# Kernel optimization log

Hardware: AMD Instinct MI355X
Metric: run time of the kernel (lower is better)

The kernel has to match this reference:

```python
import jax, jax.numpy as jnp
import numpy as np

D_MODEL = 1024
N_HEADS = 16
D_HEAD = D_MODEL // N_HEADS


def setup_inputs() -> dict:
    key = jax.random.key(0)
    ks = jax.random.split(key, 5)
    s_in = 1.0 / np.sqrt(D_MODEL)
    x = jax.random.normal(ks[0], (2, 2048, D_MODEL), dtype=jnp.float32)
    W_qkv = jax.random.uniform(ks[1], (D_MODEL, 3 * D_MODEL), jnp.float32, -s_in, s_in)
    b_qkv = jax.random.uniform(ks[2], (3 * D_MODEL,), jnp.float32, -s_in, s_in)
    W_out = jax.random.uniform(ks[3], (D_MODEL, D_MODEL), jnp.float32, -s_in, s_in)
    b_out = jax.random.uniform(ks[4], (D_MODEL,), jnp.float32, -s_in, s_in)
    return {"x": x, "W_qkv": W_qkv, "b_qkv": b_qkv, "W_out": W_out, "b_out": b_out}


def reference(x, W_qkv, b_qkv, W_out, b_out):
    B, T, C = x.shape
    qkv = x @ W_qkv + b_qkv                      # [B,T,3C]
    q, k, v = jnp.split(qkv, 3, axis=-1)
    # [B,T,C] -> [B,H,T,Dh]
    def heads(t):
        return t.reshape(B, T, N_HEADS, D_HEAD).transpose(0, 2, 1, 3)
    q, k, v = heads(q), heads(k), heads(v)
    att = jnp.einsum('bhqd,bhkd->bhqk', q, k) / np.sqrt(D_HEAD).astype(np.float32)
    causal = jnp.tril(jnp.ones((T, T), dtype=bool))  # True = keep
    att = jnp.where(causal, att, -jnp.inf)
    att = jax.nn.softmax(att, axis=-1)
    y = jnp.einsum('bhqk,bhkd->bhqd', att, v)    # [B,H,T,Dh]
    y = y.transpose(0, 2, 1, 3).reshape(B, T, C)
    y = y @ W_out + b_out
    return (y, att)
```

## Files before the change

kernel.cpp:

```cpp
#include <hip/hip_runtime.h>

#define B_ 2
#define T_ 2048
#define C_ 1024
#define H_ 16
#define DH_ 64
#define N3_ 3072
#define BT_ 4096

typedef __attribute__((ext_vector_type(4))) float f32x4;
typedef __attribute__((ext_vector_type(8))) short short8;
typedef __attribute__((ext_vector_type(4))) unsigned short us4;

__device__ __forceinline__ unsigned short f2bf(float f) {
  return __builtin_bit_cast(unsigned short, (__bf16)f);
}

__device__ __forceinline__ float bf2f(unsigned short s) {
  unsigned int u = ((unsigned int)s) << 16;
  return __builtin_bit_cast(float, u);
}

__device__ __forceinline__ void gload16(const void* g, void* l) {
  __builtin_amdgcn_global_load_lds(
      (const __attribute__((address_space(1))) unsigned int*)g,
      (__attribute__((address_space(3))) unsigned int*)l, 16, 0, 0);
}

__device__ __forceinline__ void lds_barrier() {
  asm volatile("s_waitcnt lgkmcnt(0)" ::: "memory");
  __builtin_amdgcn_s_barrier();
}

#define VM_BARRIER(N)                                        \
  do {                                                       \
    asm volatile("s_waitcnt vmcnt(" #N ")" ::: "memory");    \
    __builtin_amdgcn_s_barrier();                            \
  } while (0)

#define QSCALE 0.1803368801111137f

__global__ __launch_bounds__(256) void prep_kernel(const float* __restrict__ x,
                                                   const float* __restrict__ W_qkv,
                                                   const float* __restrict__ W_out,
                                                   unsigned short* __restrict__ xb,
                                                   unsigned short* __restrict__ wqkvT,
                                                   unsigned short* __restrict__ woutT) {
  __shared__ float tile[32][33];
  int b = blockIdx.x;
  if (b < 4096) {
    size_t i = (size_t)b * 256 + threadIdx.x;
    float4 v = *(const float4*)(x + i * 4);
    us4 o = {f2bf(v.x), f2bf(v.y), f2bf(v.z), f2bf(v.w)};
    *(us4*)(xb + i * 4) = o;
    return;
  }
  const float* W;
  unsigned short* Wt;
  int Ncols, bx, by;
  if (b < 4096 + 3072) {
    int bb = b - 4096;
    W = W_qkv; Wt = wqkvT; Ncols = 3072; bx = bb % 96; by = bb / 96;
  } else {
    int bb = b - 7168;
    W = W_out; Wt = woutT; Ncols = 1024; bx = bb % 32; by = bb / 32;
  }
  int n0 = bx * 32, k0 = by * 32;
  int tx = threadIdx.x & 31, ty = threadIdx.x >> 5;
#pragma unroll
  for (int i = 0; i < 4; ++i) {
    int k = k0 + ty + i * 8;
    tile[ty + i * 8][tx] = W[(size_t)k * Ncols + n0 + tx];
  }
  __syncthreads();
#pragma unroll
  for (int i = 0; i < 4; ++i) {
    int n = n0 + ty + i * 8;
    Wt[(size_t)n * 1024 + k0 + tx] = f2bf(tile[tx][ty + i * 8]);
  }
}

template <int MODE, int BN>
__global__ __launch_bounds__(256) void gemm_kernel(
    const unsigned short* __restrict__ A, const unsigned short* __restrict__ Bt,
    const float* __restrict__ bias, unsigned short* __restrict__ q_ws,
    unsigned short* __restrict__ k_ws, unsigned short* __restrict__ vt_ws,
    float* __restrict__ yout) {
  __shared__ unsigned short lds_a[128 * 32];
  __shared__ unsigned short lds_b[BN * 32];
  const int tid = threadIdx.x;
  const int w = tid >> 6, l = tid & 63;
  const int m0 = blockIdx.y * 128;
  const int n0 = blockIdx.x * BN;
  const int wr = (w >> 1) * 64, wc = (w & 1) * (BN / 2);
  constexpr int NI = BN / 32;
  const int K = 1024;

  f32x4 acc[4][NI] = {};
  for (int k0 = 0; k0 < K; k0 += 32) {
    __syncthreads();
#pragma unroll
    for (int i = 0; i < 2; ++i) {
      int li = i * 256 + tid;
      int row = li >> 2, cl = li & 3, cs = cl ^ (row & 3);
      gload16((const char*)A + ((size_t)(m0 + row) * K + k0) * 2 + cs * 16,
              (char*)lds_a + li * 16);
    }
#pragma unroll
    for (int i = 0; i < BN / 64; ++i) {
      int li = i * 256 + tid;
      int row = li >> 2, cl = li & 3, cs = cl ^ (row & 3);
      gload16((const char*)Bt + ((size_t)(n0 + row) * K + k0) * 2 + cs * 16,
              (char*)lds_b + li * 16);
    }
    __syncthreads();
    short8 af[4], bfr[NI];
#pragma unroll
    for (int mi = 0; mi < 4; ++mi) {
      int m = wr + mi * 16 + (l & 15);
      af[mi] = *(const short8*)((const char*)lds_a + m * 64 + (((l >> 4) ^ (m & 3)) * 16));
    }
#pragma unroll
    for (int ni = 0; ni < NI; ++ni) {
      int n = wc + ni * 16 + (l & 15);
      bfr[ni] = *(const short8*)((const char*)lds_b + n * 64 + (((l >> 4) ^ (n & 3)) * 16));
    }
#pragma unroll
    for (int mi = 0; mi < 4; ++mi)
#pragma unroll
      for (int ni = 0; ni < NI; ++ni)
        acc[mi][ni] = __builtin_amdgcn_mfma_f32_16x16x32_bf16(af[mi], bfr[ni], acc[mi][ni], 0, 0, 0);
  }

  float bi[NI];
#pragma unroll
  for (int ni = 0; ni < NI; ++ni) bi[ni] = bias[n0 + wc + ni * 16 + (l & 15)];

  if (MODE == 1) {
#pragma unroll
    for (int mi = 0; mi < 4; ++mi) {
#pragma unroll
      for (int ni = 0; ni < NI; ++ni) {
        int n = n0 + wc + ni * 16 + (l & 15);
#pragma unroll
        for (int r = 0; r < 4; ++r) {
          int m = m0 + wr + mi * 16 + ((l >> 4) << 2) + r;
          yout[(size_t)m * 1024 + n] = acc[mi][ni][r] + bi[ni];
        }
      }
    }
  } else {
    int sec = (n0 + wc) >> 10;
#pragma unroll
    for (int mi = 0; mi < 4; ++mi) {
#pragma unroll
      for (int ni = 0; ni < NI; ++ni) {
        int n = n0 + wc + ni * 16 + (l & 15);
        int nn = n & 1023, h = nn >> 6, d = nn & 63;
        if (sec == 2) {
          int mbase = m0 + wr + mi * 16 + ((l >> 4) << 2);
          int bb = mbase >> 11, t = mbase & 2047;
          us4 o;
#pragma unroll
          for (int r = 0; r < 4; ++r) o[r] = f2bf(acc[mi][ni][r] + bi[ni]);
          *(us4*)(vt_ws + ((size_t)(bb * 16 + h) * 64 + d) * 2048 + t) = o;
        } else {
#pragma unroll
          for (int r = 0; r < 4; ++r) {
            int m = m0 + wr + mi * 16 + ((l >> 4) << 2) + r;
            int bb = m >> 11, t = m & 2047;
            float v = acc[mi][ni][r] + bi[ni];
            size_t idx = ((size_t)(bb * 16 + h) * 2048 + t) * 64 + d;
            if (sec == 0)
              q_ws[idx] = f2bf(v * QSCALE);
            else
              k_ws[idx] = f2bf(v);
          }
        }
      }
    }
  }
}

__global__ __launch_bounds__(512) void attn_kernel(
    const unsigned short* __restrict__ q_ws, const unsigned short* __restrict__ k_ws,
    const unsigned short* __restrict__ vt_ws, float* __restrict__ att,
    unsigned short* __restrict__ yh) {
  __shared__ unsigned short lds_k[2][64 * 64];
  __shared__ unsigned short lds_v[2][64 * 64];
  __shared__ unsigned short lds_p[128 * 72];
  const int tid = threadIdx.x, w = tid >> 6, l = tid & 63;
  const int id = blockIdx.x;
  const int rr = id >> 8, j = id & 255;
  int qt = j & 15;
  if (rr) qt = 15 - qt;
  const int bh = (j >> 4) + (rr << 4);
  const int q0 = qt * 128;
  const size_t hoff = (size_t)bh * (2048 * 64);
  const char* kbase = (const char*)k_ws + hoff * 2;
  const char* vbase = (const char*)vt_ws + hoff * 2;

  auto stageK = [&](int kt, int buf) {
    int row = tid >> 3, cl = tid & 7, cs = cl ^ (row & 7);
    gload16(kbase + (size_t)kt * 8192 + row * 128 + cs * 16, (char*)lds_k[buf] + tid * 16);
  };
  auto stageV = [&](int kt, int buf) {
    int row = tid >> 3, cl = tid & 7, cs = cl ^ (row & 7);
    gload16(vbase + (size_t)row * 4096 + kt * 128 + cs * 16, (char*)lds_v[buf] + tid * 16);
  };

  short8 qf[2];
  {
    int row = q0 + w * 16 + (l & 15);
    const char* qb = (const char*)q_ws + (hoff + (size_t)row * 64) * 2;
    qf[0] = *(const short8*)(qb + ((l >> 4) * 16));
    qf[1] = *(const short8*)(qb + 64 + ((l >> 4) * 16));
  }

  const int rowbase = q0 + w * 16 + ((l >> 4) << 2);
  const int nkt = 2 * qt + 2;

  float lsum[4] = {0.f, 0.f, 0.f, 0.f};
  stageK(0, 0);
  VM_BARRIER(0);
  for (int kt = 0; kt < nkt; ++kt) {
    const int cur = kt & 1;
    if (kt + 1 < nkt) stageK(kt + 1, cur ^ 1);
    const bool diag = (kt >= 2 * qt);
    f32x4 s[4] = {};
    __builtin_amdgcn_s_setprio(1);
#pragma unroll
    for (int ni = 0; ni < 4; ++ni) {
      int jj = ni * 16 + (l & 15);
#pragma unroll
      for (int cc = 0; cc < 2; ++cc) {
        short8 bf = *(const short8*)((const char*)lds_k[cur] + jj * 128 +
                                     (((cc * 4 + (l >> 4)) ^ (jj & 7)) * 16));
        s[ni] = __builtin_amdgcn_mfma_f32_16x16x32_bf16(qf[cc], bf, s[ni], 0, 0, 0);
      }
    }
    __builtin_amdgcn_s_setprio(0);
#pragma unroll
    for (int ni = 0; ni < 4; ++ni) {
#pragma unroll
      for (int r = 0; r < 4; ++r) {
        float e = __builtin_exp2f(s[ni][r]);
        if (diag) {
          int colg = kt * 64 + ni * 16 + (l & 15);
          if (colg > rowbase + r) e = 0.f;
        }
        lsum[r] += e;
      }
    }
    if (kt + 1 < nkt) VM_BARRIER(0);
  }

  float invl[4];
#pragma unroll
  for (int r = 0; r < 4; ++r) {
    float t = lsum[r];
    t += __shfl_xor(t, 1);
    t += __shfl_xor(t, 2);
    t += __shfl_xor(t, 4);
    t += __shfl_xor(t, 8);
    invl[r] = 1.0f / t;
  }

  f32x4 yacc[4] = {};
  float* attb = att + (size_t)bh * 2048 * 2048;
  stageK(0, 0);
  stageV(0, 0);
  VM_BARRIER(0);
  for (int kt = 0; kt < nkt; ++kt) {
    const int cur = kt & 1;
    if (kt + 1 < nkt) { stageK(kt + 1, cur ^ 1); stageV(kt + 1, cur ^ 1); }
    const bool diag = (kt >= 2 * qt);
    f32x4 s[4] = {};
    __builtin_amdgcn_s_setprio(1);
#pragma unroll
    for (int ni = 0; ni < 4; ++ni) {
      int jj = ni * 16 + (l & 15);
#pragma unroll
      for (int cc = 0; cc < 2; ++cc) {
        short8 bf = *(const short8*)((const char*)lds_k[cur] + jj * 128 +
                                     (((cc * 4 + (l >> 4)) ^ (jj & 7)) * 16));
        s[ni] = __builtin_amdgcn_mfma_f32_16x16x32_bf16(qf[cc], bf, s[ni], 0, 0, 0);
      }
    }
    __builtin_amdgcn_s_setprio(0);
#pragma unroll
    for (int ni = 0; ni < 4; ++ni) {
#pragma unroll
      for (int r = 0; r < 4; ++r) {
        float p = __builtin_exp2f(s[ni][r]) * invl[r];
        if (diag) {
          int colg = kt * 64 + ni * 16 + (l & 15);
          if (colg > rowbase + r) p = 0.f;
        }
        lds_p[(w * 16 + ((l >> 4) << 2) + r) * 72 + ni * 16 + (l & 15)] = f2bf(p);
      }
    }
    lds_barrier();
#pragma unroll
    for (int cc = 0; cc < 2; ++cc) {
      int prow = w * 16 + (l & 15);
      short8 pf = *(const short8*)((const char*)lds_p + prow * 144 + cc * 64 + ((l >> 4) * 16));
      float* ad = attb + (size_t)(q0 + prow) * 2048 + kt * 64 + cc * 32 + ((l >> 4) * 8);
      float4 v0 = make_float4(bf2f((unsigned short)pf[0]), bf2f((unsigned short)pf[1]),
                              bf2f((unsigned short)pf[2]), bf2f((unsigned short)pf[3]));
      float4 v1 = make_float4(bf2f((unsigned short)pf[4]), bf2f((unsigned short)pf[5]),
                              bf2f((unsigned short)pf[6]), bf2f((unsigned short)pf[7]));
      *(float4*)ad = v0;
      *(float4*)(ad + 4) = v1;
      __builtin_amdgcn_s_setprio(1);
#pragma unroll
      for (int ni = 0; ni < 4; ++ni) {
        int d = ni * 16 + (l & 15);
        short8 vf = *(const short8*)((const char*)lds_v[cur] + d * 128 +
                                     (((cc * 4 + (l >> 4)) ^ (d & 7)) * 16));
        yacc[ni] = __builtin_amdgcn_mfma_f32_16x16x32_bf16(pf, vf, yacc[ni], 0, 0, 0);
      }
      __builtin_amdgcn_s_setprio(0);
    }
    if (kt + 1 < nkt) VM_BARRIER(4);
  }

  {
    int bb = bh >> 4, h = bh & 15;
#pragma unroll
    for (int ni = 0; ni < 4; ++ni) {
      int d = ni * 16 + (l & 15);
#pragma unroll
      for (int r = 0; r < 4; ++r) {
        int t = rowbase + r;
        yh[((size_t)bb * 2048 + t) * 1024 + h * 64 + d] = f2bf(yacc[ni][r]);
      }
    }
  }

  int cstart = q0 + 128;
  if (cstart < 2048) {
    int nz = 2048 - cstart;
    float4 z = make_float4(0.f, 0.f, 0.f, 0.f);
    for (int row = 0; row < 128; ++row) {
      float* dst = attb + (size_t)(q0 + row) * 2048 + cstart;
      for (int c = tid * 4; c < nz; c += 2048) *(float4*)(dst + c) = z;
    }
  }
}

extern "C" void kernel_launch(void* const* d_in, const int* in_sizes, int n_in,
                              void* d_out, int out_size, void* d_ws, size_t ws_size,
                              hipStream_t stream) {
  const float* x = (const float*)d_in[0];
  const float* W_qkv = (const float*)d_in[1];
  const float* b_qkv = (const float*)d_in[2];
  const float* W_out = (const float*)d_in[3];
  const float* b_out = (const float*)d_in[4];
  float* out = (float*)d_out;

  char* ws = (char*)d_ws;
  unsigned short* xb = (unsigned short*)(ws);
  unsigned short* wqkvT = (unsigned short*)(ws + 8388608);
  unsigned short* woutT = (unsigned short*)(ws + 14680064);
  unsigned short* q_ws = (unsigned short*)(ws + 16777216);
  unsigned short* k_ws = (unsigned short*)(ws + 25165824);
  unsigned short* vt_ws = (unsigned short*)(ws + 33554432);
  unsigned short* yh_ws = (unsigned short*)(ws + 41943040);

  float* y_out = out;
  float* att_out = out + (size_t)BT_ * C_;

  prep_kernel<<<8192, 256, 0, stream>>>(x, W_qkv, W_out, xb, wqkvT, woutT);
  gemm_kernel<0, 128><<<dim3(24, 32), 256, 0, stream>>>(xb, wqkvT, b_qkv, q_ws, k_ws, vt_ws,
                                                        nullptr);
  attn_kernel<<<512, 512, 0, stream>>>(q_ws, k_ws, vt_ws, att_out, yh_ws);
  gemm_kernel<1, 64><<<dim3(16, 32), 256, 0, stream>>>(yh_ws, woutT, b_out, nullptr, nullptr,
                                                       nullptr, y_out);
}
```

Before: 252.5 us.

## Split attention into stats and write kernels, use nontemporal stores for att

Moves the softmax row-sum pass into its own kernel that writes inverse row sums to workspace, reusing the xb region since it is dead after the QKV GEMM. The write kernel then loads those sums and does only the probability write and PV accumulation. Stores of the large attention matrix and its zero fill become nontemporal to avoid polluting cache. The split adds a kernel launch and a small global round trip but lets each kernel use fewer registers and less LDS.

```diff
diff --git a/kernel.cpp b/kernel.cpp
--- a/kernel.cpp
+++ b/kernel.cpp
@@ -182,10 +182,86 @@
   }
 }
 
-__global__ __launch_bounds__(512) void attn_kernel(
+__global__ __launch_bounds__(512) void attn_stats_kernel(
     const unsigned short* __restrict__ q_ws, const unsigned short* __restrict__ k_ws,
-    const unsigned short* __restrict__ vt_ws, float* __restrict__ att,
-    unsigned short* __restrict__ yh) {
+    float* __restrict__ invl_ws) {
+  __shared__ unsigned short lds_k[2][64 * 64];
+  const int tid = threadIdx.x, w = tid >> 6, l = tid & 63;
+  const int id = blockIdx.x;
+  const int rr = id >> 8, j = id & 255;
+  int qt = j & 15;
+  if (rr) qt = 15 - qt;
+  const int bh = (j >> 4) + (rr << 4);
+  const int q0 = qt * 128;
+  const size_t hoff = (size_t)bh * (2048 * 64);
+  const char* kbase = (const char*)k_ws + hoff * 2;
+
+  auto stageK = [&](int kt, int buf) {
+    int row = tid >> 3, cl = tid & 7, cs = cl ^ (row & 7);
+    gload16(kbase + (size_t)kt * 8192 + row * 128 + cs * 16, (char*)lds_k[buf] + tid * 16);
+  };
+
+  short8 qf[2];
+  {
+    int row = q0 + w * 16 + (l & 15);
+    const char* qb = (const char*)q_ws + (hoff + (size_t)row * 64) * 2;
+    qf[0] = *(const short8*)(qb + ((l >> 4) * 16));
+    qf[1] = *(const short8*)(qb + 64 + ((l >> 4) * 16));
+  }
+
+  const int rowbase = q0 + w * 16 + ((l >> 4) << 2);
+  const int nkt = 2 * qt + 2;
+
+  float lsum[4] = {0.f, 0.f, 0.f, 0.f};
+  stageK(0, 0);
+  VM_BARRIER(0);
+  for (int kt = 0; kt < nkt; ++kt) {
+    const int cur = kt & 1;
+    if (kt + 1 < nkt) stageK(kt + 1, cur ^ 1);
+    const bool diag = (kt >= 2 * qt);
+    f32x4 s[4] = {};
+    __builtin_amdgcn_s_setprio(1);
+#pragma unroll
+    for (int ni = 0; ni < 4; ++ni) {
+      int jj = ni * 16 + (l & 15);
+#pragma unroll
+      for (int cc = 0; cc < 2; ++cc) {
+        short8 bf = *(const short8*)((const char*)lds_k[cur] + jj * 128 +
+                                     (((cc * 4 + (l >> 4)) ^ (jj & 7)) * 16));
+        s[ni] = __builtin_amdgcn_mfma_f32_16x16x32_bf16(qf[cc], bf, s[ni], 0, 0, 0);
+      }
+    }
+    __builtin_amdgcn_s_setprio(0);
+#pragma unroll
+    for (int ni = 0; ni < 4; ++ni) {
+#pragma unroll
+      for (int r = 0; r < 4; ++r) {
+        float e = __builtin_exp2f(s[ni][r]);
+        if (diag) {
+          int colg = kt * 64 + ni * 16 + (l & 15);
+          if (colg > rowbase + r) e = 0.f;
+        }
+        lsum[r] += e;
+      }
+    }
+    if (kt + 1 < nkt) VM_BARRIER(0);
+  }
+
+#pragma unroll
+  for (int r = 0; r < 4; ++r) {
+    float t = lsum[r];
+    t += __shfl_xor(t, 1);
+    t += __shfl_xor(t, 2);
+    t += __shfl_xor(t, 4);
+    t += __shfl_xor(t, 8);
+    if ((l & 15) == 0) invl_ws[bh * 2048 + rowbase + r] = 1.0f / t;
+  }
+}
+
+__global__ __launch_bounds__(512) void attn_write_kernel(
+    const unsigned short* __restrict__ q_ws, const unsigned short* __restrict__ k_ws,
+    const unsigned short* __restrict__ vt_ws, const float* __restrict__ invl_ws,
+    float* __restrict__ att, unsigned short* __restrict__ yh) {
   __shared__ unsigned short lds_k[2][64 * 64];
   __shared__ unsigned short lds_v[2][64 * 64];
   __shared__ unsigned short lds_p[128 * 72];
@@ -220,51 +296,9 @@
   const int rowbase = q0 + w * 16 + ((l >> 4) << 2);
   const int nkt = 2 * qt + 2;
 
-  float lsum[4] = {0.f, 0.f, 0.f, 0.f};
-  stageK(0, 0);
-  VM_BARRIER(0);
-  for (int kt = 0; kt < nkt; ++kt) {
-    const int cur = kt & 1;
-    if (kt + 1 < nkt) stageK(kt + 1, cur ^ 1);
-    const bool diag = (kt >= 2 * qt);
-    f32x4 s[4] = {};
-    __builtin_amdgcn_s_setprio(1);
-#pragma unroll
-    for (int ni = 0; ni < 4; ++ni) {
-      int jj = ni * 16 + (l & 15);
-#pragma unroll
-      for (int cc = 0; cc < 2; ++cc) {
-        short8 bf = *(const short8*)((const char*)lds_k[cur] + jj * 128 +
-                                     (((cc * 4 + (l >> 4)) ^ (jj & 7)) * 16));
-        s[ni] = __builtin_amdgcn_mfma_f32_16x16x32_bf16(qf[cc], bf, s[ni], 0, 0, 0);
-      }
-    }
-    __builtin_amdgcn_s_setprio(0);
-#pragma unroll
-    for (int ni = 0; ni < 4; ++ni) {
-#pragma unroll
-      for (int r = 0; r < 4; ++r) {
-        float e = __builtin_exp2f(s[ni][r]);
-        if (diag) {
-          int colg = kt * 64 + ni * 16 + (l & 15);
-          if (colg > rowbase + r) e = 0.f;
-        }
-        lsum[r] += e;
-      }
-    }
-    if (kt + 1 < nkt) VM_BARRIER(0);
-  }
-
   float invl[4];
 #pragma unroll
-  for (int r = 0; r < 4; ++r) {
-    float t = lsum[r];
-    t += __shfl_xor(t, 1);
-    t += __shfl_xor(t, 2);
-    t += __shfl_xor(t, 4);
-    t += __shfl_xor(t, 8);
-    invl[r] = 1.0f / t;
-  }
+  for (int r = 0; r < 4; ++r) invl[r] = invl_ws[bh * 2048 + rowbase + r];
 
   f32x4 yacc[4] = {};
   float* attb = att + (size_t)bh * 2048 * 2048;
@@ -306,12 +340,12 @@
       int prow = w * 16 + (l & 15);
       short8 pf = *(const short8*)((const char*)lds_p + prow * 144 + cc * 64 + ((l >> 4) * 16));
       float* ad = attb + (size_t)(q0 + prow) * 2048 + kt * 64 + cc * 32 + ((l >> 4) * 8);
-      float4 v0 = make_float4(bf2f((unsigned short)pf[0]), bf2f((unsigned short)pf[1]),
-                              bf2f((unsigned short)pf[2]), bf2f((unsigned short)pf[3]));
-      float4 v1 = make_float4(bf2f((unsigned short)pf[4]), bf2f((unsigned short)pf[5]),
-                              bf2f((unsigned short)pf[6]), bf2f((unsigned short)pf[7]));
-      *(float4*)ad = v0;
-      *(float4*)(ad + 4) = v1;
+      f32x4 v0 = {bf2f((unsigned short)pf[0]), bf2f((unsigned short)pf[1]),
+                  bf2f((unsigned short)pf[2]), bf2f((unsigned short)pf[3])};
+      f32x4 v1 = {bf2f((unsigned short)pf[4]), bf2f((unsigned short)pf[5]),
+                  bf2f((unsigned short)pf[6]), bf2f((unsigned short)pf[7])};
+      __builtin_nontemporal_store(v0, (f32x4*)ad);
+      __builtin_nontemporal_store(v1, (f32x4*)(ad + 4));
       __builtin_amdgcn_s_setprio(1);
 #pragma unroll
       for (int ni = 0; ni < 4; ++ni) {
@@ -341,10 +375,11 @@
   int cstart = q0 + 128;
   if (cstart < 2048) {
     int nz = 2048 - cstart;
-    float4 z = make_float4(0.f, 0.f, 0.f, 0.f);
+    f32x4 z = {0.f, 0.f, 0.f, 0.f};
     for (int row = 0; row < 128; ++row) {
       float* dst = attb + (size_t)(q0 + row) * 2048 + cstart;
-      for (int c = tid * 4; c < nz; c += 2048) *(float4*)(dst + c) = z;
+      for (int c = tid * 4; c < nz; c += 2048)
+        __builtin_nontemporal_store(z, (f32x4*)(dst + c));
     }
   }
 }
@@ -361,6 +396,7 @@
 
   char* ws = (char*)d_ws;
   unsigned short* xb = (unsigned short*)(ws);
+  float* invl_ws = (float*)(ws);
   unsigned short* wqkvT = (unsigned short*)(ws + 8388608);
   unsigned short* woutT = (unsigned short*)(ws + 14680064);
   unsigned short* q_ws = (unsigned short*)(ws + 16777216);
@@ -374,7 +410,8 @@
   prep_kernel<<<8192, 256, 0, stream>>>(x, W_qkv, W_out, xb, wqkvT, woutT);
   gemm_kernel<0, 128><<<dim3(24, 32), 256, 0, stream>>>(xb, wqkvT, b_qkv, q_ws, k_ws, vt_ws,
                                                         nullptr);
-  attn_kernel<<<512, 512, 0, stream>>>(q_ws, k_ws, vt_ws, att_out, yh_ws);
+  attn_stats_kernel<<<512, 512, 0, stream>>>(q_ws, k_ws, invl_ws);
+  attn_write_kernel<<<512, 512, 0, stream>>>(q_ws, k_ws, vt_ws, invl_ws, att_out, yh_ws);
   gemm_kernel<1, 64><<<dim3(16, 32), 256, 0, stream>>>(yh_ws, woutT, b_out, nullptr, nullptr,
                                                        nullptr, y_out);
 }
```

Measured after the change: 324.4 us. +28.5%, slower.

## Use 128-wide single-buffered K/V tiles in attention instead of double-buffered 64-wide

Applied to the files above, without the earlier changes.

Widens the key tile from 64 to 128 columns so each iteration does twice the MFMA work and the loop runs half as many times. It drops the double-buffered prefetch: each iteration now barriers, loads K (and V), waits, then computes. This halves the per-tile loop and barrier count, but load latency is no longer hidden behind compute. The diagonal tile now masks more wasted work, and the P tile is written in two halves with an extra barrier.

```diff
diff --git a/kernel.cpp b/kernel.cpp
--- a/kernel.cpp
+++ b/kernel.cpp
@@ -186,8 +186,8 @@
     const unsigned short* __restrict__ q_ws, const unsigned short* __restrict__ k_ws,
     const unsigned short* __restrict__ vt_ws, float* __restrict__ att,
     unsigned short* __restrict__ yh) {
-  __shared__ unsigned short lds_k[2][64 * 64];
-  __shared__ unsigned short lds_v[2][64 * 64];
+  __shared__ unsigned short lds_k[128 * 64];
+  __shared__ unsigned short lds_v[64 * 128];
   __shared__ unsigned short lds_p[128 * 72];
   const int tid = threadIdx.x, w = tid >> 6, l = tid & 63;
   const int id = blockIdx.x;
@@ -200,13 +200,21 @@
   const char* kbase = (const char*)k_ws + hoff * 2;
   const char* vbase = (const char*)vt_ws + hoff * 2;
 
-  auto stageK = [&](int kt, int buf) {
-    int row = tid >> 3, cl = tid & 7, cs = cl ^ (row & 7);
-    gload16(kbase + (size_t)kt * 8192 + row * 128 + cs * 16, (char*)lds_k[buf] + tid * 16);
+  auto stageK = [&](int kt) {
+#pragma unroll
+    for (int i = 0; i < 2; ++i) {
+      int li = i * 512 + tid;
+      int row = li >> 3, cl = li & 7, cs = cl ^ (row & 7);
+      gload16(kbase + ((size_t)kt * 128 + row) * 128 + cs * 16, (char*)lds_k + li * 16);
+    }
   };
-  auto stageV = [&](int kt, int buf) {
-    int row = tid >> 3, cl = tid & 7, cs = cl ^ (row & 7);
-    gload16(vbase + (size_t)row * 4096 + kt * 128 + cs * 16, (char*)lds_v[buf] + tid * 16);
+  auto stageV = [&](int kt) {
+#pragma unroll
+    for (int i = 0; i < 2; ++i) {
+      int li = i * 512 + tid;
+      int row = li >> 4, cl = li & 15, cs = cl ^ (row & 15);
+      gload16(vbase + (size_t)row * 4096 + kt * 256 + cs * 16, (char*)lds_v + li * 16);
+    }
   };
 
   short8 qf[2];
@@ -218,41 +226,41 @@
   }
 
   const int rowbase = q0 + w * 16 + ((l >> 4) << 2);
-  const int nkt = 2 * qt + 2;
+  const int nkt = qt + 1;
 
   float lsum[4] = {0.f, 0.f, 0.f, 0.f};
-  stageK(0, 0);
-  VM_BARRIER(0);
   for (int kt = 0; kt < nkt; ++kt) {
-    const int cur = kt & 1;
-    if (kt + 1 < nkt) stageK(kt + 1, cur ^ 1);
-    const bool diag = (kt >= 2 * qt);
-    f32x4 s[4] = {};
+    lds_barrier();
+    stageK(kt);
+    VM_BARRIER(0);
+    const bool diag = (kt == qt);
+    f32x4 s[8];
+#pragma unroll
+    for (int ni = 0; ni < 8; ++ni) s[ni] = f32x4{0.f, 0.f, 0.f, 0.f};
     __builtin_amdgcn_s_setprio(1);
 #pragma unroll
-    for (int ni = 0; ni < 4; ++ni) {
+    for (int ni = 0; ni < 8; ++ni) {
       int jj = ni * 16 + (l & 15);
 #pragma unroll
       for (int cc = 0; cc < 2; ++cc) {
-        short8 bf = *(const short8*)((const char*)lds_k[cur] + jj * 128 +
+        short8 kf = *(const short8*)((const char*)lds_k + jj * 128 +
                                      (((cc * 4 + (l >> 4)) ^ (jj & 7)) * 16));
-        s[ni] = __builtin_amdgcn_mfma_f32_16x16x32_bf16(qf[cc], bf, s[ni], 0, 0, 0);
+        s[ni] = __builtin_amdgcn_mfma_f32_16x16x32_bf16(qf[cc], kf, s[ni], 0, 0, 0);
       }
     }
     __builtin_amdgcn_s_setprio(0);
 #pragma unroll
-    for (int ni = 0; ni < 4; ++ni) {
+    for (int ni = 0; ni < 8; ++ni) {
 #pragma unroll
       for (int r = 0; r < 4; ++r) {
         float e = __builtin_exp2f(s[ni][r]);
         if (diag) {
-          int colg = kt * 64 + ni * 16 + (l & 15);
+          int colg = kt * 128 + ni * 16 + (l & 15);
           if (colg > rowbase + r) e = 0.f;
         }
         lsum[r] += e;
       }
     }
-    if (kt + 1 < nkt) VM_BARRIER(0);
   }
 
   float invl[4];
@@ -268,61 +276,67 @@
 
   f32x4 yacc[4] = {};
   float* attb = att + (size_t)bh * 2048 * 2048;
-  stageK(0, 0);
-  stageV(0, 0);
-  VM_BARRIER(0);
   for (int kt = 0; kt < nkt; ++kt) {
-    const int cur = kt & 1;
-    if (kt + 1 < nkt) { stageK(kt + 1, cur ^ 1); stageV(kt + 1, cur ^ 1); }
-    const bool diag = (kt >= 2 * qt);
-    f32x4 s[4] = {};
+    lds_barrier();
+    stageK(kt);
+    stageV(kt);
+    VM_BARRIER(0);
+    const bool diag = (kt == qt);
+    f32x4 s[8];
+#pragma unroll
+    for (int ni = 0; ni < 8; ++ni) s[ni] = f32x4{0.f, 0.f, 0.f, 0.f};
     __builtin_amdgcn_s_setprio(1);
 #pragma unroll
-    for (int ni = 0; ni < 4; ++ni) {
+    for (int ni = 0; ni < 8; ++ni) {
       int jj = ni * 16 + (l & 15);
 #pragma unroll
       for (int cc = 0; cc < 2; ++cc) {
-        short8 bf = *(const short8*)((const char*)lds_k[cur] + jj * 128 +
+        short8 kf = *(const short8*)((const char*)lds_k + jj * 128 +
                                      (((cc * 4 + (l >> 4)) ^ (jj & 7)) * 16));
-        s[ni] = __builtin_amdgcn_mfma_f32_16x16x32_bf16(qf[cc], bf, s[ni], 0, 0, 0);
+        s[ni] = __builtin_amdgcn_mfma_f32_16x16x32_bf16(qf[cc], kf, s[ni], 0, 0, 0);
       }
     }
     __builtin_amdgcn_s_setprio(0);
 #pragma unroll
-    for (int ni = 0; ni < 4; ++ni) {
-#pragma unroll
-      for (int r = 0; r < 4; ++r) {
-        float p = __builtin_exp2f(s[ni][r]) * invl[r];
-        if (diag) {
-          int colg = kt * 64 + ni * 16 + (l & 15);
-          if (colg > rowbase + r) p = 0.f;
-        }
-        lds_p[(w * 16 + ((l >> 4) << 2) + r) * 72 + ni * 16 + (l & 15)] = f2bf(p);
-      }
-    }
-    lds_barrier();
-#pragma unroll
-    for (int cc = 0; cc < 2; ++cc) {
-      int prow = w * 16 + (l & 15);
-      short8 pf = *(const short8*)((const char*)lds_p + prow * 144 + cc * 64 + ((l >> 4) * 16));
-      float* ad = attb + (size_t)(q0 + prow) * 2048 + kt * 64 + cc * 32 + ((l >> 4) * 8);
-      float4 v0 = make_float4(bf2f((unsigned short)pf[0]), bf2f((unsigned short)pf[1]),
-                              bf2f((unsigned short)pf[2]), bf2f((unsigned short)pf[3]));
-      float4 v1 = make_float4(bf2f((unsigned short)pf[4]), bf2f((unsigned short)pf[5]),
-                              bf2f((unsigned short)pf[6]), bf2f((unsigned short)pf[7]));
-      *(float4*)ad = v0;
-      *(float4*)(ad + 4) = v1;
-      __builtin_amdgcn_s_setprio(1);
-#pragma unroll
-      for (int ni = 0; ni < 4; ++ni) {
-        int d = ni * 16 + (l & 15);
-        short8 vf = *(const short8*)((const char*)lds_v[cur] + d * 128 +
-                                     (((cc * 4 + (l >> 4)) ^ (d & 7)) * 16));
-        yacc[ni] = __builtin_amdgcn_mfma_f32_16x16x32_bf16(pf, vf, yacc[ni], 0, 0, 0);
-      }
-      __builtin_amdgcn_s_setprio(0);
-    }
-    if (kt + 1 < nkt) VM_BARRIER(4);
+    for (int h = 0; h < 2; ++h) {
+      if (h) lds_barrier();
+#pragma unroll
+      for (int nl = 0; nl < 4; ++nl) {
+        int ni = h * 4 + nl;
+#pragma unroll
+        for (int r = 0; r < 4; ++r) {
+          float p = __builtin_exp2f(s[ni][r]) * invl[r];
+          if (diag) {
+            int colg = kt * 128 + ni * 16 + (l & 15);
+            if (colg > rowbase + r) p = 0.f;
+          }
+          lds_p[(w * 16 + ((l >> 4) << 2) + r) * 72 + nl * 16 + (l & 15)] = f2bf(p);
+        }
+      }
+      lds_barrier();
+#pragma unroll
+      for (int cc = 0; cc < 2; ++cc) {
+        int prow = w * 16 + (l & 15);
+        short8 pf = *(const short8*)((const char*)lds_p + prow * 144 + cc * 64 + ((l >> 4) * 16));
+        float* ad = attb + (size_t)(q0 + prow) * 2048 + kt * 128 + h * 64 + cc * 32 + ((l >> 4) * 8);
+        float4 v0 = make_float4(bf2f((unsigned short)pf[0]), bf2f((unsigned short)pf[1]),
+                                bf2f((unsigned short)pf[2]), bf2f((unsigned short)pf[3]));
+        float4 v1 = make_float4(bf2f((unsigned short)pf[4]), bf2f((unsigned short)pf[5]),
+                                bf2f((unsigned short)pf[6]), bf2f((unsigned short)pf[7]));
+        *(float4*)ad = v0;
+        *(float4*)(ad + 4) = v1;
+        __builtin_amdgcn_s_setprio(1);
+        int kc = h * 2 + cc;
+#pragma unroll
+        for (int ni = 0; ni < 4; ++ni) {
+          int d = ni * 16 + (l & 15);
+          short8 vf = *(const short8*)((const char*)lds_v + d * 256 +
+                                       (((kc * 4 + (l >> 4)) ^ (d & 15)) * 16));
+          yacc[ni] = __builtin_amdgcn_mfma_f32_16x16x32_bf16(pf, vf, yacc[ni], 0, 0, 0);
+        }
+        __builtin_amdgcn_s_setprio(0);
+      }
+    }
   }
 
   {
```

After: 262.6 us. +4.0%, slower.
